# Performance work log

Measured on AMD Instinct MI355X. Metric: run time of the kernel, lower is better.

## Reference

```python
import jax, jax.numpy as jnp
import numpy as np

NUM_HEADS = 8
HEAD_DIM = 128
ATTN_SCALE = 0.12


def _rotary_tables(T, head_dim, dtype=jnp.float32):
    # modded-nanogpt half-truncated RoPE: rotate only first half of freq slots
    quarter = head_dim // 4
    angular = (1.0 / 1024.0) ** jnp.linspace(0.0, 1.0, quarter, dtype=dtype)
    angular = jnp.concatenate([angular, jnp.zeros(quarter, dtype=dtype)])  # [head_dim//2]
    t = jnp.arange(T, dtype=dtype)
    theta = t[:, None] * angular[None, :]  # [T, head_dim//2]
    return jnp.cos(theta), jnp.sin(theta)


def _apply_rotary(x, cos, sin):
    # x: [B, T, H, D]; cos/sin: [T, D//2]
    x1, x2 = jnp.split(x, 2, axis=-1)
    c = cos[None, :, None, :]
    s = sin[None, :, None, :]
    y1 = x1 * c + x2 * s
    y2 = -x1 * s + x2 * c
    return jnp.concatenate([y1, y2], axis=-1)


def _rms_norm(x):
    eps = jnp.asarray(jnp.finfo(x.dtype).eps, x.dtype)
    var = jnp.mean(jnp.square(x), axis=-1, keepdims=True)
    return x * jax.lax.rsqrt(var + eps)


def setup_inputs() -> dict:
    key = jax.random.key(0)
    k1, k2, k3, k4, k5 = jax.random.split(key, 5)
    B, T, D = 1, 4096, 1024
    hdim = NUM_HEADS * HEAD_DIM
    std = 0.5 * D ** (-0.5)
    x = jax.random.normal(k1, (B, T, D), dtype=jnp.float32)
    ve = jax.random.normal(k2, (B, T, hdim), dtype=jnp.float32)
    qkv_w = jax.random.normal(k3, (3, hdim, D), dtype=jnp.float32) * std
    lambdas = jnp.array([0.5, 0.5], dtype=jnp.float32)
    c_proj_w = jax.random.normal(k5, (D, hdim), dtype=jnp.float32) * std
    return {"x": x, "ve": ve, "qkv_w": qkv_w, "lambdas": lambdas, "c_proj_w": c_proj_w}


def reference(x, ve, qkv_w, lambdas, c_proj_w):
    B, T, D = x.shape
    H, Hd = NUM_HEADS, HEAD_DIM
    # QKV projection: qkv_w [3, H*Hd, D]
    qkv = jnp.einsum('btd,ckd->btck', x, qkv_w)  # [B, T, 3, H*Hd]
    qkv = qkv.reshape(B, T, 3, H, Hd)
    q, k, v = qkv[:, :, 0], qkv[:, :, 1], qkv[:, :, 2]  # [B, T, H, Hd]
    # QK RMSNorm
    q = _rms_norm(q)
    k = _rms_norm(k)
    # RoPE
    cos, sin = _rotary_tables(T, Hd, dtype=x.dtype)
    q = _apply_rotary(q, cos, sin)
    k = _apply_rotary(k, cos, sin)
    # value-embedding lambda mix
    v = lambdas[0] * v + lambdas[1] * ve.reshape(B, T, H, Hd)
    # causal attention with fixed scale 0.12 (block-causal FlexAttention mask)
    scores = jnp.einsum('bthd,bshd->bhts', q, k) * ATTN_SCALE  # [B, H, T, T]
    causal = jnp.tril(jnp.ones((T, T), dtype=bool))
    scores = jnp.where(causal[None, None], scores, jnp.asarray(-jnp.inf, scores.dtype))
    probs = jax.nn.softmax(scores, axis=-1)
    y = jnp.einsum('bhts,bshd->bthd', probs, v)  # [B, T, H, Hd]
    y = y.reshape(B, T, H * Hd)
    return y @ c_proj_w.T  # [B, T, D]
```

## Files before the change

### kernel.cpp

```cpp
#include <hip/hip_runtime.h>

typedef __bf16 bf16;
typedef __bf16 bf16x8 __attribute__((ext_vector_type(8)));
typedef __bf16 bf16x4 __attribute__((ext_vector_type(4)));
typedef __bf16 bf16x2 __attribute__((ext_vector_type(2)));
typedef float f32x4 __attribute__((ext_vector_type(4)));
typedef float f32x16 __attribute__((ext_vector_type(16)));
typedef int i32x4 __attribute__((ext_vector_type(4)));
typedef int i32x2 __attribute__((ext_vector_type(2)));

#define GLL16(gp, lp)                                                          \
  __builtin_amdgcn_global_load_lds(                                            \
      (const __attribute__((address_space(1))) unsigned int*)(gp),             \
      (__attribute__((address_space(3))) unsigned int*)(lp), 16, 0, 0)

__global__ __launch_bounds__(256) void cast3_f32_bf16(
    const float* __restrict__ a, bf16* __restrict__ oa, int na4,
    const float* __restrict__ b, bf16* __restrict__ ob, int nb4,
    const float* __restrict__ c, bf16* __restrict__ oc, int nc4) {
  int i = blockIdx.x * blockDim.x + threadIdx.x;
  int stride = gridDim.x * blockDim.x;
  int total = na4 + nb4 + nc4;
  for (; i < total; i += stride) {
    const float4* src;
    bf16x4* dst;
    int j = i;
    if (j < na4) {
      src = (const float4*)a + j; dst = (bf16x4*)oa + j;
    } else if ((j -= na4) < nb4) {
      src = (const float4*)b + j; dst = (bf16x4*)ob + j;
    } else {
      j -= nb4;
      src = (const float4*)c + j; dst = (bf16x4*)oc + j;
    }
    float4 v = *src;
    bf16x4 o;
    o[0] = (bf16)v.x; o[1] = (bf16)v.y; o[2] = (bf16)v.z; o[3] = (bf16)v.w;
    *dst = o;
  }
}

template <int K, int LDC, int BM, typename CT>
__global__ __launch_bounds__(256) void gemm_bt(
    const bf16* __restrict__ A, const bf16* __restrict__ B,
    CT* __restrict__ C) {
  __shared__ __align__(16) bf16 As[BM * 64];
  __shared__ __align__(16) bf16 Bs[128 * 64];
  const int tid  = threadIdx.x;
  const int lane = tid & 63;
  const int wave = tid >> 6;
  const int ln15 = lane & 15, quad = lane >> 4;
  const int wm = wave >> 1, wn = wave & 1;
  const int m0 = blockIdx.y * BM, n0 = blockIdx.x * 128;
  constexpr int MI = BM / 32;

  f32x4 acc[MI][4] = {};

  for (int k0 = 0; k0 < K; k0 += 64) {
    __syncthreads();
#pragma unroll
    for (int j = 0; j < BM / 32; ++j) {
      int gbase = j * 256 + wave * 64;
      int g = gbase + lane;
      int r = g >> 3, c = (g & 7) ^ (r & 7);
      GLL16(A + (size_t)(m0 + r) * K + k0 + c * 8, As + (size_t)gbase * 8);
    }
#pragma unroll
    for (int j = 0; j < 4; ++j) {
      int gbase = j * 256 + wave * 64;
      int g = gbase + lane;
      int r = g >> 3, c = (g & 7) ^ (r & 7);
      GLL16(B + (size_t)(n0 + r) * K + k0 + c * 8, Bs + (size_t)gbase * 8);
    }
    __syncthreads();
#pragma unroll
    for (int kk = 0; kk < 2; ++kk) {
      bf16x8 af[MI], bfr[4];
#pragma unroll
      for (int mi = 0; mi < MI; ++mi) {
        int m = wm * (BM / 2) + mi * 16 + ln15;
        int cg = kk * 4 + quad;
        af[mi] = *(const bf16x8*)(As + (m * 8 + (cg ^ (m & 7))) * 8);
      }
#pragma unroll
      for (int ni = 0; ni < 4; ++ni) {
        int n = wn * 64 + ni * 16 + ln15;
        int cg = kk * 4 + quad;
        bfr[ni] = *(const bf16x8*)(Bs + (n * 8 + (cg ^ (n & 7))) * 8);
      }
#pragma unroll
      for (int mi = 0; mi < MI; ++mi)
#pragma unroll
        for (int ni = 0; ni < 4; ++ni)
          acc[mi][ni] = __builtin_amdgcn_mfma_f32_16x16x32_bf16(
              af[mi], bfr[ni], acc[mi][ni], 0, 0, 0);
    }
  }
#pragma unroll
  for (int mi = 0; mi < MI; ++mi)
#pragma unroll
    for (int ni = 0; ni < 4; ++ni)
#pragma unroll
      for (int r = 0; r < 4; ++r) {
        int row = m0 + wm * (BM / 2) + mi * 16 + quad * 4 + r;
        int col = n0 + wn * 64 + ni * 16 + ln15;
        C[(size_t)row * LDC + col] = (CT)acc[mi][ni][r];
      }
}

__global__ __launch_bounds__(256) void qkv_post(
    const bf16* __restrict__ qkv, const float* __restrict__ ve,
    const float* __restrict__ lambdas, bf16* __restrict__ qn,
    bf16* __restrict__ kn, bf16* __restrict__ vt) {
  const int h  = blockIdx.x;
  const int t0 = blockIdx.y * 64;
  const int tid = threadIdx.x;
  const int wave = tid >> 6, lane = tid & 63;
  const int l31 = lane & 31, hl = lane >> 5;
  __shared__ __align__(16) float tile[64][129];

  const int d0 = 2 * l31 + 64 * hl;
  const int trow0 = t0 + wave * 16;
  float ca0 = 1.f, sa0 = 0.f, ca1 = 1.f, sa1 = 0.f;
  float c0 = 1.f, s0 = 0.f, c1 = 1.f, s1 = 0.f;
  if (l31 < 16) {
    float a0 = exp2f((float)(2 * l31) * (-10.0f / 31.0f));
    float a1 = exp2f((float)(2 * l31 + 1) * (-10.0f / 31.0f));
    __sincosf(a0, &sa0, &ca0);
    __sincosf(a1, &sa1, &ca1);
    __sincosf((float)trow0 * a0, &s0, &c0);
    __sincosf((float)trow0 * a1, &s1, &c1);
  }

  for (int i = 0; i < 16; ++i) {
    int t = trow0 + i;
    float s0m = hl ? -s0 : s0;
    float s1m = hl ? -s1 : s1;
#pragma unroll
    for (int qk = 0; qk < 2; ++qk) {
      const bf16* row = qkv + (size_t)t * 3072 + qk * 1024 + h * 128;
      bf16x2 xp = *(const bf16x2*)(row + d0);
      float xa = (float)xp[0], xb = (float)xp[1];
      float ss = xa * xa + xb * xb;
#pragma unroll
      for (int m = 1; m < 64; m <<= 1) ss += __shfl_xor(ss, m, 64);
      float rinv = rsqrtf(ss * (1.0f / 128.0f) + 1.1920929e-7f);
      if (qk == 0) rinv *= 0.12f;
      float pa = __shfl_xor(xa, 32, 64);
      float pb = __shfl_xor(xb, 32, 64);
      float ya = (xa * c0 + pa * s0m) * rinv;
      float yb = (xb * c1 + pb * s1m) * rinv;
      bf16* orow = (qk == 0 ? qn : kn) + (size_t)t * 1024 + h * 128;
      bf16x2 o; o[0] = (bf16)ya; o[1] = (bf16)yb;
      *(bf16x2*)(orow + d0) = o;
    }
    float nc0 = c0 * ca0 - s0 * sa0, ns0 = s0 * ca0 + c0 * sa0;
    float nc1 = c1 * ca1 - s1 * sa1, ns1 = s1 * ca1 + c1 * sa1;
    c0 = nc0; s0 = ns0; c1 = nc1; s1 = ns1;
  }

  float l0 = lambdas[0], l1 = lambdas[1];
  for (int c = 0; c < 16; ++c) {
    int idx = c * 512 + tid * 2;
    int d = idx & 127, tl = idx >> 7;
    int t = t0 + tl;
    bf16x2 vp = *(const bf16x2*)(qkv + (size_t)t * 3072 + 2048 + h * 128 + d);
    float2 vev = *(const float2*)(ve + (size_t)t * 1024 + h * 128 + d);
    tile[tl][d]     = l0 * (float)vp[0] + l1 * vev.x;
    tile[tl][d + 1] = l0 * (float)vp[1] + l1 * vev.y;
  }
  __syncthreads();
  for (int c = 0; c < 16; ++c) {
    int idx = c * 512 + tid * 2;
    int tl = idx & 63, d = idx >> 6;
    bf16x2 o;
    o[0] = (bf16)tile[tl][d];
    o[1] = (bf16)tile[tl + 1][d];
    *(bf16x2*)(vt + ((size_t)(h * 128 + d)) * 4096 + t0 + tl) = o;
  }
}

__global__ __launch_bounds__(256, 2) void flash_attn(
    const bf16* __restrict__ qn, const bf16* __restrict__ kn,
    const bf16* __restrict__ vt, float* __restrict__ Op,
    float* __restrict__ ls) {
  const int id = blockIdx.x;
  const int qt = (id < 256) ? (31 - (id >> 4)) : ((id - 256) >> 4);
  const int sub = id & 15;
  const int h = sub >> 1;
  const int half = sub & 1;
  const int tid = threadIdx.x;
  const int wave = tid >> 6, lane = tid & 63;
  const int l31 = lane & 31, hl = lane >> 5;

  __shared__ __align__(16) bf16 smem[4 * 64 * 128];
  bf16* Ks = smem;
  bf16* Vs = smem + 2 * 64 * 128;

  const int nkv = 2 * (qt + 1);
  const int half0 = qt + 1;
  const int kt_begin = half ? half0 : 0;
  const int kt_end = half ? nkv : half0;
  const int niter = kt_end - kt_begin;
  const int pidx = (h * 32 + qt) * 2 + half;

  const int qminw = qt * 128 + wave * 32;
  const int qg = qminw + l31;

  bf16x8 qf[8];
  {
    const bf16* qb = qn + (size_t)qg * 1024 + h * 128 + hl * 8;
#pragma unroll
    for (int f = 0; f < 8; ++f) qf[f] = *(const bf16x8*)(qb + f * 16);
  }

  f32x16 acc_o[4] = {};
  float rs = 0.0f;

  auto prefetch = [&](int kt, int buf) {
    const int kv0 = kt * 64;
    bf16* ks = Ks + buf * (64 * 128);
    bf16* vs = Vs + buf * (128 * 64);
#pragma unroll
    for (int jj = 0; jj < 4; ++jj) {
      int gbase = jj * 256 + wave * 64;
      int g = gbase + lane;
      int r = g >> 4, c = (g & 15) ^ (r & 15);
      GLL16(kn + (size_t)(kv0 + r) * 1024 + h * 128 + c * 8,
            ks + (size_t)gbase * 8);
    }
#pragma unroll
    for (int jj = 0; jj < 4; ++jj) {
      int gbase = jj * 256 + wave * 64;
      int g = gbase + lane;
      int d = g >> 3, c = (g & 7) ^ (d & 7);
      GLL16(vt + ((size_t)(h * 128 + d)) * 4096 + kv0 + c * 8,
            vs + (size_t)gbase * 8);
    }
  };

  prefetch(kt_begin, 0);

  for (int it = 0; it < niter; ++it) {
    const int kt = kt_begin + it;
    const int kv0 = kt * 64;
    __syncthreads();
    if (it + 1 < niter) prefetch(kt + 1, (it + 1) & 1);
    const bf16* ksb = Ks + (it & 1) * (64 * 128);
    const bf16* vsb = Vs + (it & 1) * (128 * 64);

    if (kv0 > qminw + 31) continue;

    f32x16 acc0 = {}, acc1 = {};
    const int l15 = l31 & 15;
    __builtin_amdgcn_s_setprio(1);
#pragma unroll
    for (int f = 0; f < 8; ++f) {
      bf16x8 a0 = *(const bf16x8*)(
          ksb + (l31 * 16 + ((2 * f + hl) ^ l15)) * 8);
      bf16x8 a1 = *(const bf16x8*)(
          ksb + ((32 + l31) * 16 + ((2 * f + hl) ^ l15)) * 8);
      acc0 = __builtin_amdgcn_mfma_f32_32x32x16_bf16(a0, qf[f], acc0, 0, 0, 0);
      acc1 = __builtin_amdgcn_mfma_f32_32x32x16_bf16(a1, qf[f], acc1, 0, 0, 0);
    }
    __builtin_amdgcn_s_setprio(0);

    const bool needmask = (kv0 + 63 > qminw);
    float rsp[4] = {0.f, 0.f, 0.f, 0.f};
    if (needmask) {
#pragma unroll
      for (int rr = 0; rr < 16; ++rr) {
        int kvl = (rr & 3) + 8 * (rr >> 2) + 4 * hl;
        float v0 = __expf(acc0[rr]);
        float v1 = __expf(acc1[rr]);
        if (kv0 + kvl > qg) v0 = 0.0f;
        if (kv0 + 32 + kvl > qg) v1 = 0.0f;
        acc0[rr] = v0; acc1[rr] = v1;
        rsp[rr & 3] += v0 + v1;
      }
    } else {
#pragma unroll
      for (int rr = 0; rr < 16; ++rr) {
        float v0 = __expf(acc0[rr]);
        float v1 = __expf(acc1[rr]);
        acc0[rr] = v0; acc1[rr] = v1;
        rsp[rr & 3] += v0 + v1;
      }
    }
    rs += (rsp[0] + rsp[1]) + (rsp[2] + rsp[3]);

    int pk0[8], pk1[8];
#pragma unroll
    for (int g = 0; g < 8; ++g) {
      bf16x2 t0, t1;
      t0[0] = (bf16)acc0[2 * g]; t0[1] = (bf16)acc0[2 * g + 1];
      t1[0] = (bf16)acc1[2 * g]; t1[1] = (bf16)acc1[2 * g + 1];
      pk0[g] = __builtin_bit_cast(int, t0);
      pk1[g] = __builtin_bit_cast(int, t1);
    }

    bf16x8 pf[4];
#if __has_builtin(__builtin_amdgcn_permlane32_swap)
#pragma unroll
    for (int cc = 0; cc < 4; ++cc) {
      int s0 = (cc < 2) ? pk0[(cc & 1) * 4 + 0] : pk1[(cc & 1) * 4 + 0];
      int s1 = (cc < 2) ? pk0[(cc & 1) * 4 + 1] : pk1[(cc & 1) * 4 + 1];
      int s2 = (cc < 2) ? pk0[(cc & 1) * 4 + 2] : pk1[(cc & 1) * 4 + 2];
      int s3 = (cc < 2) ? pk0[(cc & 1) * 4 + 3] : pk1[(cc & 1) * 4 + 3];
      i32x2 r02 = __builtin_amdgcn_permlane32_swap(s0, s2, false, false);
      i32x2 r13 = __builtin_amdgcn_permlane32_swap(s1, s3, false, false);
      i32x4 dv;
      dv[0] = r02[0];
      dv[1] = r13[0];
      dv[2] = r02[1];
      dv[3] = r13[1];
      pf[cc] = __builtin_bit_cast(bf16x8, dv);
    }
#else
#pragma unroll
    for (int cc = 0; cc < 4; ++cc) {
      int s0 = (cc < 2) ? pk0[(cc & 1) * 4 + 0] : pk1[(cc & 1) * 4 + 0];
      int s1 = (cc < 2) ? pk0[(cc & 1) * 4 + 1] : pk1[(cc & 1) * 4 + 1];
      int s2 = (cc < 2) ? pk0[(cc & 1) * 4 + 2] : pk1[(cc & 1) * 4 + 2];
      int s3 = (cc < 2) ? pk0[(cc & 1) * 4 + 3] : pk1[(cc & 1) * 4 + 3];
      int sh0 = __shfl_xor(s0, 32, 64);
      int sh1 = __shfl_xor(s1, 32, 64);
      int sh2 = __shfl_xor(s2, 32, 64);
      int sh3 = __shfl_xor(s3, 32, 64);
      int own0 = hl ? s2 : s0;
      int own1 = hl ? s3 : s1;
      int par0 = hl ? sh2 : sh0;
      int par1 = hl ? sh3 : sh1;
      i32x4 dv;
      dv[0] = hl ? par0 : own0;
      dv[1] = hl ? par1 : own1;
      dv[2] = hl ? own0 : par0;
      dv[3] = hl ? own1 : par1;
      pf[cc] = __builtin_bit_cast(bf16x8, dv);
    }
#endif

    __builtin_amdgcn_s_setprio(1);
#pragma unroll
    for (int dt = 0; dt < 4; ++dt) {
      int vrow = dt * 32 + l31;
#pragma unroll
      for (int cc = 0; cc < 4; ++cc) {
        bf16x8 a = *(const bf16x8*)(
            vsb + (vrow * 8 + ((2 * cc + hl) ^ (vrow & 7))) * 8);
        acc_o[dt] =
            __builtin_amdgcn_mfma_f32_32x32x16_bf16(a, pf[cc], acc_o[dt], 0, 0, 0);
      }
    }
    __builtin_amdgcn_s_setprio(0);
  }

  rs += __shfl_xor(rs, 32, 64);
  if (hl == 0) ls[pidx * 128 + wave * 32 + l31] = rs;
  float* opb = Op + (size_t)pidx * 16384 + (size_t)(wave * 32 + l31) * 128;
#pragma unroll
  for (int dt = 0; dt < 4; ++dt)
#pragma unroll
    for (int rg = 0; rg < 4; ++rg) {
      float4 o;
      o.x = acc_o[dt][rg * 4 + 0];
      o.y = acc_o[dt][rg * 4 + 1];
      o.z = acc_o[dt][rg * 4 + 2];
      o.w = acc_o[dt][rg * 4 + 3];
      int d0 = dt * 32 + 4 * hl + 8 * rg;
      *(float4*)(opb + d0) = o;
    }
}

__global__ __launch_bounds__(256) void attn_combine(
    const float* __restrict__ Op, const float* __restrict__ ls,
    bf16* __restrict__ y) {
  int gid = blockIdx.x * 256 + threadIdx.x;
  int t = gid >> 8;
  int c4 = gid & 255;
  int qt = t >> 7, ql = t & 127;
  int h = c4 >> 5;
  int d = (c4 & 31) * 4;
  int pb = (h * 32 + qt) * 2;
  const float4 o0 = *(const float4*)(Op + (size_t)pb * 16384 + ql * 128 + d);
  const float4 o1 =
      *(const float4*)(Op + (size_t)(pb + 1) * 16384 + ql * 128 + d);
  float inv = 1.0f / (ls[pb * 128 + ql] + ls[(pb + 1) * 128 + ql]);
  bf16x4 o;
  o[0] = (bf16)((o0.x + o1.x) * inv);
  o[1] = (bf16)((o0.y + o1.y) * inv);
  o[2] = (bf16)((o0.z + o1.z) * inv);
  o[3] = (bf16)((o0.w + o1.w) * inv);
  *(bf16x4*)(y + (size_t)t * 1024 + h * 128 + d) = o;
}

extern "C" void kernel_launch(void* const* d_in, const int* in_sizes, int n_in,
                              void* d_out, int out_size, void* d_ws,
                              size_t ws_size, hipStream_t stream) {
  const float* x       = (const float*)d_in[0];
  const float* ve      = (const float*)d_in[1];
  const float* qkv_w   = (const float*)d_in[2];
  const float* lambdas = (const float*)d_in[3];
  const float* c_proj  = (const float*)d_in[4];
  float* out = (float*)d_out;

  char* ws = (char*)d_ws;
  bf16* qkv   = (bf16*)ws;
  bf16* xbf   = (bf16*)(ws + 25165824);
  bf16* wqkv  = (bf16*)(ws + 33554432);
  bf16* wproj = (bf16*)(ws + 39845888);
  bf16* qn    = (bf16*)(ws + 41943040);
  bf16* kn    = (bf16*)(ws + 50331648);
  bf16* vt    = (bf16*)(ws + 58720256);
  bf16* yb    = (bf16*)(ws + 67108864);
  float* Op  = (float*)ws;
  float* lsw = (float*)(ws + 33554432);

  cast3_f32_bf16<<<2048, 256, 0, stream>>>(x, xbf, 4194304 / 4, qkv_w, wqkv,
                                           3145728 / 4, c_proj, wproj,
                                           1048576 / 4);

  gemm_bt<1024, 3072, 128, bf16><<<dim3(24, 32), 256, 0, stream>>>(xbf, wqkv,
                                                                   qkv);

  qkv_post<<<dim3(8, 64), 256, 0, stream>>>(qkv, ve, lambdas, qn, kn, vt);

  flash_attn<<<512, 256, 0, stream>>>(qn, kn, vt, Op, lsw);
  attn_combine<<<4096, 256, 0, stream>>>(Op, lsw, yb);

  gemm_bt<1024, 1024, 64, float><<<dim3(8, 64), 256, 0, stream>>>(yb, wproj,
                                                                  out);
}
```

Before: 223.8 us.

## Fuse split-KV combine into flash attention and remap GEMM blocks across XCDs

The separate attn_combine kernel is removed. The second of each pair of split-KV flash_attn blocks to finish, detected through an atomic counter reset in qkv_post, now merges the two partial outputs and writes the bf16 result. This saves a kernel launch and the round-trip through the fused-away pass. Separately, the GEMM grid is flattened and block IDs are swizzled so consecutive tiles on the same XCD share operand rows, aiming for better L2 reuse. The change relies on threadfence/atomic ordering and on the counter being reset each call.

```diff
diff --git a/kernel.cpp b/kernel.cpp
--- a/kernel.cpp
+++ b/kernel.cpp
@@ -40,7 +40,7 @@
   }
 }
 
-template <int K, int LDC, int BM, typename CT>
+template <int K, int LDC, int BM, int NBX, typename CT>
 __global__ __launch_bounds__(256) void gemm_bt(
     const bf16* __restrict__ A, const bf16* __restrict__ B,
     CT* __restrict__ C) {
@@ -51,7 +51,9 @@
   const int wave = tid >> 6;
   const int ln15 = lane & 15, quad = lane >> 4;
   const int wm = wave >> 1, wn = wave & 1;
-  const int m0 = blockIdx.y * BM, n0 = blockIdx.x * 128;
+  const int flat = blockIdx.x;
+  const int wg = (flat & 7) * (gridDim.x >> 3) + (flat >> 3);
+  const int m0 = (wg / NBX) * BM, n0 = (wg % NBX) * 128;
   constexpr int MI = BM / 32;
 
   f32x4 acc[MI][4] = {};
@@ -111,13 +113,15 @@
 __global__ __launch_bounds__(256) void qkv_post(
     const bf16* __restrict__ qkv, const float* __restrict__ ve,
     const float* __restrict__ lambdas, bf16* __restrict__ qn,
-    bf16* __restrict__ kn, bf16* __restrict__ vt) {
+    bf16* __restrict__ kn, bf16* __restrict__ vt, int* __restrict__ cnt) {
   const int h  = blockIdx.x;
   const int t0 = blockIdx.y * 64;
   const int tid = threadIdx.x;
   const int wave = tid >> 6, lane = tid & 63;
   const int l31 = lane & 31, hl = lane >> 5;
   __shared__ __align__(16) float tile[64][129];
+
+  if (h == 0 && blockIdx.y == 0) cnt[tid] = 0;
 
   const int d0 = 2 * l31 + 64 * hl;
   const int trow0 = t0 + wave * 16;
@@ -149,9 +153,9 @@
       float pa = __shfl_xor(xa, 32, 64);
       float pb = __shfl_xor(xb, 32, 64);
       float ya = (xa * c0 + pa * s0m) * rinv;
-      float yb = (xb * c1 + pb * s1m) * rinv;
+      float yb2 = (xb * c1 + pb * s1m) * rinv;
       bf16* orow = (qk == 0 ? qn : kn) + (size_t)t * 1024 + h * 128;
-      bf16x2 o; o[0] = (bf16)ya; o[1] = (bf16)yb;
+      bf16x2 o; o[0] = (bf16)ya; o[1] = (bf16)yb2;
       *(bf16x2*)(orow + d0) = o;
     }
     float nc0 = c0 * ca0 - s0 * sa0, ns0 = s0 * ca0 + c0 * sa0;
@@ -183,7 +187,7 @@
 __global__ __launch_bounds__(256, 2) void flash_attn(
     const bf16* __restrict__ qn, const bf16* __restrict__ kn,
     const bf16* __restrict__ vt, float* __restrict__ Op,
-    float* __restrict__ ls) {
+    float* __restrict__ ls, int* __restrict__ cnt, bf16* __restrict__ yb) {
   const int id = blockIdx.x;
   const int qt = (id < 256) ? (31 - (id >> 4)) : ((id - 256) >> 4);
   const int sub = id & 15;
@@ -370,28 +374,31 @@
       int d0 = dt * 32 + 4 * hl + 8 * rg;
       *(float4*)(opb + d0) = o;
     }
-}
-
-__global__ __launch_bounds__(256) void attn_combine(
-    const float* __restrict__ Op, const float* __restrict__ ls,
-    bf16* __restrict__ y) {
-  int gid = blockIdx.x * 256 + threadIdx.x;
-  int t = gid >> 8;
-  int c4 = gid & 255;
-  int qt = t >> 7, ql = t & 127;
-  int h = c4 >> 5;
-  int d = (c4 & 31) * 4;
-  int pb = (h * 32 + qt) * 2;
-  const float4 o0 = *(const float4*)(Op + (size_t)pb * 16384 + ql * 128 + d);
-  const float4 o1 =
-      *(const float4*)(Op + (size_t)(pb + 1) * 16384 + ql * 128 + d);
-  float inv = 1.0f / (ls[pb * 128 + ql] + ls[(pb + 1) * 128 + ql]);
-  bf16x4 o;
-  o[0] = (bf16)((o0.x + o1.x) * inv);
-  o[1] = (bf16)((o0.y + o1.y) * inv);
-  o[2] = (bf16)((o0.z + o1.z) * inv);
-  o[3] = (bf16)((o0.w + o1.w) * inv);
-  *(bf16x4*)(y + (size_t)t * 1024 + h * 128 + d) = o;
+
+  __threadfence();
+  __shared__ int lastflag;
+  if (tid == 0) lastflag = (atomicAdd(&cnt[pidx >> 1], 1) == 1);
+  __syncthreads();
+  if (!lastflag) return;
+  __threadfence();
+  const int pb = pidx & ~1;
+  const float* op0 = Op + (size_t)pb * 16384;
+  const float* op1 = Op + (size_t)(pb + 1) * 16384;
+#pragma unroll
+  for (int c = 0; c < 16; ++c) {
+    int idx = c * 256 + tid;
+    int ql = idx >> 5;
+    int d4 = (idx & 31) * 4;
+    float4 o0 = *(const float4*)(op0 + ql * 128 + d4);
+    float4 o1 = *(const float4*)(op1 + ql * 128 + d4);
+    float inv = 1.0f / (ls[pb * 128 + ql] + ls[(pb + 1) * 128 + ql]);
+    bf16x4 ov;
+    ov[0] = (bf16)((o0.x + o1.x) * inv);
+    ov[1] = (bf16)((o0.y + o1.y) * inv);
+    ov[2] = (bf16)((o0.z + o1.z) * inv);
+    ov[3] = (bf16)((o0.w + o1.w) * inv);
+    *(bf16x4*)(yb + (size_t)(qt * 128 + ql) * 1024 + h * 128 + d4) = ov;
+  }
 }
 
 extern "C" void kernel_launch(void* const* d_in, const int* in_sizes, int n_in,
@@ -415,19 +422,17 @@
   bf16* yb    = (bf16*)(ws + 67108864);
   float* Op  = (float*)ws;
   float* lsw = (float*)(ws + 33554432);
+  int*   cnt = (int*)(ws + 33816576);
 
   cast3_f32_bf16<<<2048, 256, 0, stream>>>(x, xbf, 4194304 / 4, qkv_w, wqkv,
                                            3145728 / 4, c_proj, wproj,
                                            1048576 / 4);
 
-  gemm_bt<1024, 3072, 128, bf16><<<dim3(24, 32), 256, 0, stream>>>(xbf, wqkv,
-                                                                   qkv);
-
-  qkv_post<<<dim3(8, 64), 256, 0, stream>>>(qkv, ve, lambdas, qn, kn, vt);
-
-  flash_attn<<<512, 256, 0, stream>>>(qn, kn, vt, Op, lsw);
-  attn_combine<<<4096, 256, 0, stream>>>(Op, lsw, yb);
-
-  gemm_bt<1024, 1024, 64, float><<<dim3(8, 64), 256, 0, stream>>>(yb, wproj,
-                                                                  out);
+  gemm_bt<1024, 3072, 128, 24, bf16><<<768, 256, 0, stream>>>(xbf, wqkv, qkv);
+
+  qkv_post<<<dim3(8, 64), 256, 0, stream>>>(qkv, ve, lambdas, qn, kn, vt, cnt);
+
+  flash_attn<<<512, 256, 0, stream>>>(qn, kn, vt, Op, lsw, cnt, yb);
+
+  gemm_bt<1024, 1024, 64, 8, float><<<512, 256, 0, stream>>>(yb, wproj, out);
 }
```

Measured after the change: 354.7 us. 1.58x slower.

## Fuse QK RMSNorm, RoPE and value-embedding mix into QKV GEMM epilogue

Applied to the files above, without the earlier changes.

Replaces the separate QKV GEMM and qkv_post kernels with a single GEMM whose epilogue stages the 128x128 output tile in LDS and applies RMSNorm plus RoPE for Q/K or the lambda mix plus transpose for V. This removes the round trip of the bf16 QKV intermediate through global memory and one kernel launch. The workspace layout is reshuffled to drop the intermediate buffer. In exchange the epilogue adds per-element sincos calls and scalar bf16 stores, which may reduce GEMM efficiency.

```diff
diff --git a/kernel.cpp b/kernel.cpp
--- a/kernel.cpp
+++ b/kernel.cpp
@@ -108,75 +108,125 @@
       }
 }
 
-__global__ __launch_bounds__(256) void qkv_post(
-    const bf16* __restrict__ qkv, const float* __restrict__ ve,
-    const float* __restrict__ lambdas, bf16* __restrict__ qn,
-    bf16* __restrict__ kn, bf16* __restrict__ vt) {
-  const int h  = blockIdx.x;
-  const int t0 = blockIdx.y * 64;
-  const int tid = threadIdx.x;
-  const int wave = tid >> 6, lane = tid & 63;
-  const int l31 = lane & 31, hl = lane >> 5;
-  __shared__ __align__(16) float tile[64][129];
-
-  const int d0 = 2 * l31 + 64 * hl;
-  const int trow0 = t0 + wave * 16;
-  float ca0 = 1.f, sa0 = 0.f, ca1 = 1.f, sa1 = 0.f;
-  float c0 = 1.f, s0 = 0.f, c1 = 1.f, s1 = 0.f;
-  if (l31 < 16) {
-    float a0 = exp2f((float)(2 * l31) * (-10.0f / 31.0f));
-    float a1 = exp2f((float)(2 * l31 + 1) * (-10.0f / 31.0f));
-    __sincosf(a0, &sa0, &ca0);
-    __sincosf(a1, &sa1, &ca1);
-    __sincosf((float)trow0 * a0, &s0, &c0);
-    __sincosf((float)trow0 * a1, &s1, &c1);
-  }
-
-  for (int i = 0; i < 16; ++i) {
-    int t = trow0 + i;
-    float s0m = hl ? -s0 : s0;
-    float s1m = hl ? -s1 : s1;
-#pragma unroll
-    for (int qk = 0; qk < 2; ++qk) {
-      const bf16* row = qkv + (size_t)t * 3072 + qk * 1024 + h * 128;
-      bf16x2 xp = *(const bf16x2*)(row + d0);
-      float xa = (float)xp[0], xb = (float)xp[1];
-      float ss = xa * xa + xb * xb;
+__global__ __launch_bounds__(256) void gemm_qkv(
+    const bf16* __restrict__ A, const bf16* __restrict__ B,
+    const float* __restrict__ ve, const float* __restrict__ lmb,
+    bf16* __restrict__ qn, bf16* __restrict__ kn, bf16* __restrict__ vt) {
+  __shared__ __align__(16) bf16 smem[128 * 131];
+  bf16* As = smem;
+  bf16* Bs = smem + 8192;
+  const int tid  = threadIdx.x;
+  const int lane = tid & 63;
+  const int wave = tid >> 6;
+  const int ln15 = lane & 15, quad = lane >> 4;
+  const int wm = wave >> 1, wn = wave & 1;
+  const int m0 = blockIdx.y * 128, n0 = blockIdx.x * 128;
+
+  f32x4 acc[4][4] = {};
+
+  for (int k0 = 0; k0 < 1024; k0 += 64) {
+    __syncthreads();
+#pragma unroll
+    for (int j = 0; j < 4; ++j) {
+      int gbase = j * 256 + wave * 64;
+      int g = gbase + lane;
+      int r = g >> 3, c = (g & 7) ^ (r & 7);
+      GLL16(A + (size_t)(m0 + r) * 1024 + k0 + c * 8, As + (size_t)gbase * 8);
+    }
+#pragma unroll
+    for (int j = 0; j < 4; ++j) {
+      int gbase = j * 256 + wave * 64;
+      int g = gbase + lane;
+      int r = g >> 3, c = (g & 7) ^ (r & 7);
+      GLL16(B + (size_t)(n0 + r) * 1024 + k0 + c * 8, Bs + (size_t)gbase * 8);
+    }
+    __syncthreads();
+#pragma unroll
+    for (int kk = 0; kk < 2; ++kk) {
+      bf16x8 af[4], bfr[4];
+#pragma unroll
+      for (int mi = 0; mi < 4; ++mi) {
+        int m = wm * 64 + mi * 16 + ln15;
+        int cg = kk * 4 + quad;
+        af[mi] = *(const bf16x8*)(As + (m * 8 + (cg ^ (m & 7))) * 8);
+      }
+#pragma unroll
+      for (int ni = 0; ni < 4; ++ni) {
+        int n = wn * 64 + ni * 16 + ln15;
+        int cg = kk * 4 + quad;
+        bfr[ni] = *(const bf16x8*)(Bs + (n * 8 + (cg ^ (n & 7))) * 8);
+      }
+#pragma unroll
+      for (int mi = 0; mi < 4; ++mi)
+#pragma unroll
+        for (int ni = 0; ni < 4; ++ni)
+          acc[mi][ni] = __builtin_amdgcn_mfma_f32_16x16x32_bf16(
+              af[mi], bfr[ni], acc[mi][ni], 0, 0, 0);
+    }
+  }
+
+  __syncthreads();
+  bf16* tile = smem;
+#pragma unroll
+  for (int mi = 0; mi < 4; ++mi)
+#pragma unroll
+    for (int ni = 0; ni < 4; ++ni)
+#pragma unroll
+      for (int r = 0; r < 4; ++r) {
+        int row = wm * 64 + mi * 16 + quad * 4 + r;
+        int col = wn * 64 + ni * 16 + ln15;
+        tile[row * 130 + col] = (bf16)acc[mi][ni][r];
+      }
+  __syncthreads();
+
+  const int ck = n0 >> 10;
+  const int h  = (n0 >> 7) & 7;
+
+  if (ck < 2) {
+    const int j = lane;
+    bf16* outb = (ck == 0 ? qn : kn);
+    float ang = 0.f;
+    if (j < 32) ang = exp2f((float)j * (-10.0f / 31.0f));
+    for (int i = 0; i < 32; ++i) {
+      int row = wave * 32 + i;
+      int t = m0 + row;
+      float x1 = (float)tile[row * 130 + j];
+      float x2 = (float)tile[row * 130 + j + 64];
+      float ss = x1 * x1 + x2 * x2;
 #pragma unroll
       for (int m = 1; m < 64; m <<= 1) ss += __shfl_xor(ss, m, 64);
       float rinv = rsqrtf(ss * (1.0f / 128.0f) + 1.1920929e-7f);
-      if (qk == 0) rinv *= 0.12f;
-      float pa = __shfl_xor(xa, 32, 64);
-      float pb = __shfl_xor(xb, 32, 64);
-      float ya = (xa * c0 + pa * s0m) * rinv;
-      float yb = (xb * c1 + pb * s1m) * rinv;
-      bf16* orow = (qk == 0 ? qn : kn) + (size_t)t * 1024 + h * 128;
-      bf16x2 o; o[0] = (bf16)ya; o[1] = (bf16)yb;
-      *(bf16x2*)(orow + d0) = o;
-    }
-    float nc0 = c0 * ca0 - s0 * sa0, ns0 = s0 * ca0 + c0 * sa0;
-    float nc1 = c1 * ca1 - s1 * sa1, ns1 = s1 * ca1 + c1 * sa1;
-    c0 = nc0; s0 = ns0; c1 = nc1; s1 = ns1;
-  }
-
-  float l0 = lambdas[0], l1 = lambdas[1];
-  for (int c = 0; c < 16; ++c) {
-    int idx = c * 512 + tid * 2;
-    int d = idx & 127, tl = idx >> 7;
-    int t = t0 + tl;
-    bf16x2 vp = *(const bf16x2*)(qkv + (size_t)t * 3072 + 2048 + h * 128 + d);
-    float2 vev = *(const float2*)(ve + (size_t)t * 1024 + h * 128 + d);
-    tile[tl][d]     = l0 * (float)vp[0] + l1 * vev.x;
-    tile[tl][d + 1] = l0 * (float)vp[1] + l1 * vev.y;
-  }
-  __syncthreads();
-  for (int c = 0; c < 16; ++c) {
-    int idx = c * 512 + tid * 2;
-    int tl = idx & 63, d = idx >> 6;
-    bf16x2 o;
-    o[0] = (bf16)tile[tl][d];
-    o[1] = (bf16)tile[tl + 1][d];
-    *(bf16x2*)(vt + ((size_t)(h * 128 + d)) * 4096 + t0 + tl) = o;
+      if (ck == 0) rinv *= 0.12f;
+      float c = 1.0f, s = 0.0f;
+      if (j < 32) __sincosf((float)t * ang, &s, &c);
+      float y1 = (x1 * c + x2 * s) * rinv;
+      float y2 = (x2 * c - x1 * s) * rinv;
+      bf16* orow = outb + (size_t)t * 1024 + h * 128;
+      orow[j] = (bf16)y1;
+      orow[j + 64] = (bf16)y2;
+    }
+  } else {
+    float l0 = lmb[0], l1 = lmb[1];
+    for (int c = 0; c < 32; ++c) {
+      int idx = c * 512 + tid * 2;
+      int d = idx & 127, tl = idx >> 7;
+      int t = m0 + tl;
+      bf16x2 vp = *(bf16x2*)(tile + tl * 130 + d);
+      float2 vev = *(const float2*)(ve + (size_t)t * 1024 + h * 128 + d);
+      bf16x2 o;
+      o[0] = (bf16)(l0 * (float)vp[0] + l1 * vev.x);
+      o[1] = (bf16)(l0 * (float)vp[1] + l1 * vev.y);
+      *(bf16x2*)(tile + tl * 130 + d) = o;
+    }
+    __syncthreads();
+    for (int c = 0; c < 32; ++c) {
+      int idx = c * 512 + tid * 2;
+      int tl = idx & 127, d = idx >> 7;
+      bf16x2 o;
+      o[0] = tile[tl * 130 + d];
+      o[1] = tile[(tl + 1) * 130 + d];
+      *(bf16x2*)(vt + ((size_t)(h * 128 + d)) * 4096 + m0 + tl) = o;
+    }
   }
 }
 
@@ -405,25 +455,22 @@
   float* out = (float*)d_out;
 
   char* ws = (char*)d_ws;
-  bf16* qkv   = (bf16*)ws;
-  bf16* xbf   = (bf16*)(ws + 25165824);
-  bf16* wqkv  = (bf16*)(ws + 33554432);
-  bf16* wproj = (bf16*)(ws + 39845888);
-  bf16* qn    = (bf16*)(ws + 41943040);
-  bf16* kn    = (bf16*)(ws + 50331648);
-  bf16* vt    = (bf16*)(ws + 58720256);
-  bf16* yb    = (bf16*)(ws + 67108864);
+  bf16* xbf   = (bf16*)ws;
+  bf16* wqkv  = (bf16*)(ws + 8388608);
   float* Op  = (float*)ws;
   float* lsw = (float*)(ws + 33554432);
+  bf16* wproj = (bf16*)(ws + 33816576);
+  bf16* qn    = (bf16*)(ws + 35913728);
+  bf16* kn    = (bf16*)(ws + 44302336);
+  bf16* vt    = (bf16*)(ws + 52690944);
+  bf16* yb    = (bf16*)(ws + 61079552);
 
   cast3_f32_bf16<<<2048, 256, 0, stream>>>(x, xbf, 4194304 / 4, qkv_w, wqkv,
                                            3145728 / 4, c_proj, wproj,
                                            1048576 / 4);
 
-  gemm_bt<1024, 3072, 128, bf16><<<dim3(24, 32), 256, 0, stream>>>(xbf, wqkv,
-                                                                   qkv);
-
-  qkv_post<<<dim3(8, 64), 256, 0, stream>>>(qkv, ve, lambdas, qn, kn, vt);
+  gemm_qkv<<<dim3(24, 32), 256, 0, stream>>>(xbf, wqkv, ve, lambdas, qn, kn,
+                                             vt);
 
   flash_attn<<<512, 256, 0, stream>>>(qn, kn, vt, Op, lsw);
   attn_combine<<<4096, 256, 0, stream>>>(Op, lsw, yb);
```

Result: faster. 218.2 us (-2.5%).
